# Optimization experiments

Measured on AMD Instinct MI355X. Metric: run time of the kernel, lower is better.

The kernel has to match this reference:

```python
import jax, jax.numpy as jnp
import numpy as np

N_FRAMES = 4
HEADS = 8
SEQ = 576
DIM = 640


def setup_inputs() -> dict:
    key = jax.random.key(0)
    ks = jax.random.split(key, 6)
    x = jax.random.normal(ks[0], (3 * N_FRAMES, SEQ, DIM), dtype=jnp.float32)
    s = 1.0 / np.sqrt(DIM)
    Wq = jax.random.normal(ks[1], (DIM, DIM), dtype=jnp.float32) * s
    Wk = jax.random.normal(ks[2], (DIM, DIM), dtype=jnp.float32) * s
    Wv = jax.random.normal(ks[3], (DIM, DIM), dtype=jnp.float32) * s
    Wo = jax.random.normal(ks[4], (DIM, DIM), dtype=jnp.float32) * s
    bo = jnp.zeros((DIM,), dtype=jnp.float32)
    return {"x": x, "Wq": Wq, "Wk": Wk, "Wv": Wv, "Wo": Wo, "bo": bo}


def reference(x, Wq, Wk, Wv, Wo, bo):
    # x: [3F, S, D] -- stacked [source | uncond | cond] frame batches
    B, S, D = x.shape
    n = B // 3                       # n_frames
    h = HEADS
    hd = D // h
    scale = 1.0 / jnp.sqrt(jnp.asarray(hd, x.dtype))

    # torch nn.Linear: y = x @ W.T
    q = jnp.einsum('bsd,ed->bse', x, Wq)
    k = jnp.einsum('bsd,ed->bse', x, Wk)
    v = jnp.einsum('bsd,ed->bse', x, Wv)

    def heads_fd(t):  # [F,S,D] -> [F,h,S,hd]
        return t.reshape(t.shape[0], S, h, hd).transpose(0, 2, 1, 3)

    def heads_flat(t):  # [F,S,D] -> [h, F*S, hd]  (shared across all query frames)
        return t.reshape(t.shape[0] * S, h, hd).transpose(1, 0, 2)

    # ---- source: per-frame self-attention ----
    qs, ks_, vs = heads_fd(q[:n]), heads_fd(k[:n]), heads_fd(v[:n])
    sim_s = jnp.einsum('fhqd,fhkd->fhqk', qs, ks_) * scale
    out_s = jnp.einsum('fhqk,fhkd->fhqd', jax.nn.softmax(sim_s, axis=-1), vs)

    # ---- uncond / cond: each frame attends to concatenated KV of all frames ----
    def cross_frame(q_chunk, k_chunk, v_chunk):
        qf = heads_fd(q_chunk)          # [F,h,S,hd]
        kf = heads_flat(k_chunk)        # [h,F*S,hd]
        vf = heads_flat(v_chunk)        # [h,F*S,hd]
        sim = jnp.einsum('fhqd,hkd->fhqk', qf, kf) * scale   # [F,h,S,F*S]
        return jnp.einsum('fhqk,hkd->fhqd', jax.nn.softmax(sim, axis=-1), vf)

    out_u = cross_frame(q[n:2 * n], k[n:2 * n], v[n:2 * n])
    out_c = cross_frame(q[2 * n:], k[2 * n:], v[2 * n:])

    out = jnp.concatenate([out_s, out_u, out_c], axis=0)      # [3F,h,S,hd]
    out = out.transpose(0, 2, 1, 3).reshape(B, S, D)          # merge heads
    return jnp.einsum('bsd,ed->bse', out, Wo) + bo
```

## Files before the change

kernel.cpp:

```cpp
#include <hip/hip_runtime.h>
#include <hip/hip_bf16.h>

#define SEQ    576
#define DIM    640
#define HEADS  8
#define HD     80
#define NF     4
#define NB     12
#define M_TOT  (NB * SEQ)
#define SCALE  0.11180339887498949f
#define LOG2E  1.4426950408889634f

typedef __attribute__((ext_vector_type(8))) short          bf16x8;
typedef __attribute__((ext_vector_type(4))) float          f32x4;
typedef __attribute__((ext_vector_type(8))) unsigned short u16x8;
typedef __attribute__((ext_vector_type(4))) unsigned short u16x4;

__device__ __forceinline__ unsigned short f2bf(float x) {
    unsigned u = __float_as_uint(x);
    u += 0x7fffu + ((u >> 16) & 1u);
    return (unsigned short)(u >> 16);
}
__device__ __forceinline__ float bf2f(unsigned short h) {
    return __uint_as_float((unsigned)h << 16);
}
__device__ __forceinline__ f32x4 mfma16(bf16x8 a, bf16x8 b, f32x4 c) {
    return __builtin_amdgcn_mfma_f32_16x16x32_bf16(a, b, c, 0, 0, 0);
}
__device__ __forceinline__ float fexp2(float x) {
    return __builtin_amdgcn_exp2f(x);
}
__device__ __forceinline__ void dma16(const void* g, void* s) {
    __builtin_amdgcn_global_load_lds(
        (const __attribute__((address_space(1))) void*)g,
        (__attribute__((address_space(3))) void*)s, 16, 0, 0);
}

__global__ __launch_bounds__(256) void split_kernel(
    const float* __restrict__ X,  const float* __restrict__ Wq,
    const float* __restrict__ Wk, const float* __restrict__ Wv,
    const float* __restrict__ Wo,
    unsigned short* __restrict__ Xh,  unsigned short* __restrict__ Wqh,
    unsigned short* __restrict__ Wkh, unsigned short* __restrict__ Wvh,
    unsigned short* __restrict__ Woh)
{
    const int z = blockIdx.y;
    const float* src; unsigned short* dh; int n; float s = 1.0f;
    switch (z) {
        case 0:  src = X;  dh = Xh;  n = M_TOT * DIM; break;
        case 1:  src = Wq; dh = Wqh; n = DIM * DIM; s = SCALE * LOG2E; break;
        case 2:  src = Wk; dh = Wkh; n = DIM * DIM; break;
        case 3:  src = Wv; dh = Wvh; n = DIM * DIM; break;
        default: src = Wo; dh = Woh; n = DIM * DIM; break;
    }
    const int base = blockIdx.x * 4096 + threadIdx.x * 16;
    if (base >= n) return;
#pragma unroll
    for (int half = 0; half < 2; ++half) {
        const int b = base + half * 8;
        float4 a4 = *(const float4*)(src + b);
        float4 b4 = *(const float4*)(src + b + 4);
        float vv[8] = {a4.x, a4.y, a4.z, a4.w, b4.x, b4.y, b4.z, b4.w};
        union { unsigned short u[8]; u16x8 v; } ph;
#pragma unroll
        for (int j = 0; j < 8; ++j) ph.u[j] = f2bf(vv[j] * s);
        *(u16x8*)(dh + b) = ph.v;
    }
}

__global__ __launch_bounds__(256) void qkv_mfma_kernel(
    const unsigned short* __restrict__ Xh,
    const unsigned short* __restrict__ Wqh, const unsigned short* __restrict__ Wkh,
    const unsigned short* __restrict__ Wvh,
    unsigned short* __restrict__ Qh,
    unsigned short* __restrict__ Kb, unsigned short* __restrict__ VtG)
{
    __shared__ unsigned short smem[10240];
    unsigned short* As = smem;
    unsigned short* Bs = smem + 8192;

    const int flat = blockIdx.x + 27 * (blockIdx.y + 10 * blockIdx.z);
    const int xcd  = flat & 7;
    const int slot = flat >> 3;
    const int l    = (xcd < 2 ? xcd * 102 : 204 + (xcd - 2) * 101) + slot;
    const int m_idx = l / 30;
    const int rem   = l - m_idx * 30;
    const int z     = rem / 10;
    const int n_idx = rem - z * 10;

    const unsigned short* WH = (z == 0) ? Wqh : ((z == 1) ? Wkh : Wvh);
    const int m0 = m_idx * 256;
    const int n0 = n_idx * 64;

    const int t    = threadIdx.x;
    const int w    = t >> 6;
    const int lane = t & 63;
    const int quad = lane >> 4;
    const int ln   = lane & 15;

    f32x4 acc[4][4];
#pragma unroll
    for (int mi = 0; mi < 4; ++mi)
#pragma unroll
        for (int nt = 0; nt < 4; ++nt)
#pragma unroll
            for (int e = 0; e < 4; ++e) acc[mi][nt][e] = 0.f;

    const int lr = lane >> 2;
    const int lc = (lane & 3) * 8;

    for (int k0 = 0; k0 < DIM; k0 += 32) {
        __syncthreads();
        {
            const unsigned short* gp = Xh + (size_t)(m0 + w * 64 + lr) * DIM + k0 + lc;
#pragma unroll
            for (int i = 0; i < 4; ++i)
                dma16(gp + (size_t)i * 16 * DIM, &As[(w * 64 + i * 16) * 32]);
            const size_t gb = (size_t)(n0 + w * 16 + lr) * DIM + k0 + lc;
            dma16(WH + gb, &Bs[w * 16 * 32]);
        }
        __syncthreads();

        bf16x8 af[4];
#pragma unroll
        for (int mi = 0; mi < 4; ++mi)
            af[mi] = *(const bf16x8*)&As[(w * 64 + mi * 16 + ln) * 32 + quad * 8];
#pragma unroll
        for (int nt = 0; nt < 4; ++nt) {
            bf16x8 bh = *(const bf16x8*)&Bs[(nt * 16 + ln) * 32 + quad * 8];
#pragma unroll
            for (int mi = 0; mi < 4; ++mi)
                acc[mi][nt] = mfma16(af[mi], bh, acc[mi][nt]);
        }
    }

    if (z == 0) {
#pragma unroll
        for (int mi = 0; mi < 4; ++mi)
#pragma unroll
            for (int r = 0; r < 4; ++r) {
                const size_t row = m0 + w * 64 + mi * 16 + quad * 4 + r;
#pragma unroll
                for (int nt = 0; nt < 4; ++nt)
                    Qh[row * DIM + n0 + nt * 16 + ln] = f2bf(acc[mi][nt][r]);
            }
    } else if (z == 1) {
#pragma unroll
        for (int mi = 0; mi < 4; ++mi)
#pragma unroll
            for (int r = 0; r < 4; ++r) {
                const size_t row = m0 + w * 64 + mi * 16 + quad * 4 + r;
#pragma unroll
                for (int nt = 0; nt < 4; ++nt)
                    Kb[row * DIM + n0 + nt * 16 + ln] = f2bf(acc[mi][nt][r]);
            }
    } else {
        unsigned short* Vts = smem;
#pragma unroll 1
        for (int half = 0; half < 2; ++half) {
            __syncthreads();
            if ((w >> 1) == half) {
                const int wl = w & 1;
#pragma unroll
                for (int mi = 0; mi < 4; ++mi)
#pragma unroll
                    for (int nt = 0; nt < 4; ++nt)
#pragma unroll
                        for (int r = 0; r < 4; ++r)
                            Vts[(nt * 16 + ln) * 136 + wl * 64 + mi * 16 + quad * 4 + r] =
                                f2bf(acc[mi][nt][r]);
            }
            __syncthreads();
            const int nn = t & 63;
            const int c0 = (t >> 6) * 32;
#pragma unroll
            for (int i = 0; i < 4; ++i)
                *(u16x8*)(VtG + (size_t)(n0 + nn) * M_TOT + m0 + half * 128 + c0 + i * 8) =
                    *(const u16x8*)&Vts[nn * 136 + c0 + i * 8];
        }
    }
}

__global__ __launch_bounds__(256, 2) void attn_mfma_kernel(
    const unsigned short* __restrict__ Qh,
    const unsigned short* __restrict__ Kb, const unsigned short* __restrict__ Vt,
    unsigned short* __restrict__ Oh,
    unsigned short* __restrict__ Pn, float2* __restrict__ ml)
{
    const int flat = blockIdx.x + 3 * (blockIdx.y + 8 * blockIdx.z);
    const int h    = flat & 7;
    const int slot = flat >> 3;
    const int z    = slot / 3;
    const int qt   = slot - z * 3;

    int f, kbase, nkt, idx = -1;
    if (z < 16) {
        idx = z;
        const int fi = z >> 1;
        f = 4 + fi;
        kbase = ((fi < 4 ? 4 : 8) + (z & 1) * 2) * SEQ;
        nkt = 18;
    } else {
        f = z - 16;
        kbase = f * SEQ;
        nkt = 9;
    }

    const int t    = threadIdx.x;
    const int w    = t >> 6;
    const int lane = t & 63;
    const int quad = lane >> 4;
    const int ln   = lane & 15;

    __shared__ unsigned short KhS[64 * 96];
    __shared__ unsigned short VtS[80 * 64];
    __shared__ unsigned short Pb[4 * 48 * 72];

    bf16x8 qf[3][3];
#pragma unroll
    for (int mi = 0; mi < 3; ++mi) {
        const int qrow = f * SEQ + qt * 192 + w * 48 + mi * 16 + ln;
        const unsigned short* qp = Qh + (size_t)qrow * DIM + h * HD;
#pragma unroll
        for (int kc = 0; kc < 3; ++kc) {
            const int dbase = kc * 32 + quad * 8;
            if (dbase < HD) {
                qf[mi][kc] = *(const bf16x8*)(qp + dbase);
            } else {
                union { unsigned short u[8]; bf16x8 v; } zz;
#pragma unroll
                for (int j = 0; j < 8; ++j) zz.u[j] = 0;
                qf[mi][kc] = zz.v;
            }
        }
    }

    float m_[3], l_[3];
#pragma unroll
    for (int mi = 0; mi < 3; ++mi) { m_[mi] = -INFINITY; l_[mi] = 0.f; }

    f32x4 oacc[3][5];
#pragma unroll
    for (int mi = 0; mi < 3; ++mi)
#pragma unroll
        for (int nt = 0; nt < 5; ++nt)
#pragma unroll
            for (int e = 0; e < 4; ++e) oacc[mi][nt][e] = 0.f;

    unsigned short* PbW = &Pb[w * 48 * 72];

    for (int kt = 0; kt < nkt; ++kt) {
        __syncthreads();
        {
            const unsigned short* kg = Kb + (size_t)(kbase + kt * 64) * DIM + h * HD;
#pragma unroll
            for (int rnd = 0; rnd < 3; ++rnd) {
                const int unit = rnd * 256 + t;
                const int kr = unit / 12, kc = unit % 12;
                dma16(kg + (size_t)kr * DIM + kc * 8,
                      &KhS[(rnd * 256 + w * 64) * 8]);
            }
        }
        {
#pragma unroll
            for (int u = t; u < 640; u += 256) {
                const int d = u >> 3, c8 = u & 7;
                const int c8s = (c8 + 3 * d) & 7;
                *(u16x8*)&VtS[d * 64 + c8s * 8] =
                    *(const u16x8*)(Vt + (size_t)(h * HD + d) * M_TOT +
                                    kbase + kt * 64 + c8 * 8);
            }
        }
        __syncthreads();

        f32x4 sacc[3][4];
#pragma unroll
        for (int mi = 0; mi < 3; ++mi)
#pragma unroll
            for (int nt = 0; nt < 4; ++nt)
#pragma unroll
                for (int e = 0; e < 4; ++e) sacc[mi][nt][e] = 0.f;
#pragma unroll
        for (int nt = 0; nt < 4; ++nt)
#pragma unroll
            for (int kc = 0; kc < 3; ++kc) {
                bf16x8 kf = *(const bf16x8*)&KhS[(nt * 16 + ln) * 96 + kc * 32 + quad * 8];
#pragma unroll
                for (int mi = 0; mi < 3; ++mi)
                    sacc[mi][nt] = mfma16(kf, qf[mi][kc], sacc[mi][nt]);
            }

        float aq[3];
#pragma unroll
        for (int mi = 0; mi < 3; ++mi) {
            float mx = sacc[mi][0][0];
#pragma unroll
            for (int nt = 0; nt < 4; ++nt)
#pragma unroll
                for (int r = 0; r < 4; ++r) mx = fmaxf(mx, sacc[mi][nt][r]);
            mx = fmaxf(mx, __shfl_xor(mx, 16));
            mx = fmaxf(mx, __shfl_xor(mx, 32));
            const float mnew = fmaxf(m_[mi], mx);
            aq[mi] = fexp2(m_[mi] - mnew);
            m_[mi] = mnew;
            float s = 0.f;
#pragma unroll
            for (int nt = 0; nt < 4; ++nt) {
                union { unsigned short u[4]; u16x4 v; } pk;
#pragma unroll
                for (int r = 0; r < 4; ++r) {
                    const float p = fexp2(sacc[mi][nt][r] - m_[mi]);
                    s += p;
                    pk.u[r] = (unsigned short)(__float_as_uint(p) >> 16);
                }
                *(u16x4*)&PbW[(mi * 16 + ln) * 72 + nt * 16 + quad * 4] = pk.v;
            }
            s += __shfl_xor(s, 16);
            s += __shfl_xor(s, 32);
            l_[mi] = l_[mi] * aq[mi] + s;
        }

#pragma unroll
        for (int mi = 0; mi < 3; ++mi)
#pragma unroll
            for (int r = 0; r < 4; ++r) {
                const float ar = __shfl(aq[mi], quad * 4 + r, 64);
#pragma unroll
                for (int nt = 0; nt < 5; ++nt) oacc[mi][nt][r] *= ar;
            }

        __threadfence_block();

#pragma unroll
        for (int kc = 0; kc < 2; ++kc) {
            bf16x8 pf[3];
#pragma unroll
            for (int mi = 0; mi < 3; ++mi)
                pf[mi] = *(const bf16x8*)&PbW[(mi * 16 + ln) * 72 + kc * 32 + quad * 8];
#pragma unroll
            for (int nt = 0; nt < 5; ++nt) {
                const int vrow = nt * 16 + ln;
                const int c8r  = ((kc * 4 + quad) + 3 * vrow) & 7;
                bf16x8 vf = *(const bf16x8*)&VtS[vrow * 64 + c8r * 8];
#pragma unroll
                for (int mi = 0; mi < 3; ++mi)
                    oacc[mi][nt] = mfma16(pf[mi], vf, oacc[mi][nt]);
            }
        }
    }

#pragma unroll
    for (int mi = 0; mi < 3; ++mi)
#pragma unroll
        for (int r = 0; r < 4; ++r) {
            const float lr_ = __shfl(l_[mi], quad * 4 + r, 64);
            const float inv = 1.f / lr_;
            const int rr = qt * 192 + w * 48 + mi * 16 + quad * 4 + r;
            if (idx < 0) {
                const size_t orow = (size_t)f * SEQ + rr;
#pragma unroll
                for (int nt = 0; nt < 5; ++nt)
                    Oh[orow * DIM + h * HD + nt * 16 + ln] = f2bf(oacc[mi][nt][r] * inv);
            } else {
#pragma unroll
                for (int nt = 0; nt < 5; ++nt)
                    Pn[((size_t)idx * SEQ + rr) * DIM + h * HD + nt * 16 + ln] =
                        f2bf(oacc[mi][nt][r] * inv);
            }
        }
    if (idx >= 0 && lane < 16) {
#pragma unroll
        for (int mi = 0; mi < 3; ++mi) {
            const int rr = qt * 192 + w * 48 + mi * 16 + lane;
            ml[((size_t)idx * 8 + h) * SEQ + rr] = make_float2(m_[mi], l_[mi]);
        }
    }
}

__global__ __launch_bounds__(320) void merge_kernel(
    const unsigned short* __restrict__ Pn, const float2* __restrict__ ml,
    unsigned short* __restrict__ Oh)
{
    const int row = blockIdx.x;
    const int fi  = blockIdx.y;
    const int t   = threadIdx.x;
    const int i0  = fi * 2, i1 = i0 + 1;
#pragma unroll
    for (int rep = 0; rep < 2; ++rep) {
        const int col = t + rep * 320;
        const int h = col / 80;
        const float2 a = ml[((size_t)i0 * 8 + h) * SEQ + row];
        const float2 b = ml[((size_t)i1 * 8 + h) * SEQ + row];
        const float M  = fmaxf(a.x, b.x);
        const float w0 = fexp2(a.x - M) * a.y;
        const float w1 = fexp2(b.x - M) * b.y;
        const float inv = 1.f / (w0 + w1);
        const float p0 = bf2f(Pn[((size_t)i0 * SEQ + row) * DIM + col]);
        const float p1 = bf2f(Pn[((size_t)i1 * SEQ + row) * DIM + col]);
        Oh[((size_t)(4 + fi) * SEQ + row) * DIM + col] = f2bf((w0 * p0 + w1 * p1) * inv);
    }
}

__global__ __launch_bounds__(256) void oproj_mfma_kernel(
    const unsigned short* __restrict__ Oh,
    const unsigned short* __restrict__ Woh,
    const float* __restrict__ bo, float* __restrict__ out)
{
    __shared__ unsigned short smem[10240];
    unsigned short* As = smem;
    unsigned short* Bs = smem + 8192;

    const int flat = blockIdx.x + 27 * blockIdx.y;
    const int xcd  = flat & 7;
    const int slot = flat >> 3;
    const int l    = (xcd < 6 ? xcd * 34 : 204 + (xcd - 6) * 33) + slot;
    const int m_idx = l / 10;
    const int n_idx = l - m_idx * 10;
    const int m0 = m_idx * 256;
    const int n0 = n_idx * 64;

    const int t    = threadIdx.x;
    const int w    = t >> 6;
    const int lane = t & 63;
    const int quad = lane >> 4;
    const int ln   = lane & 15;

    f32x4 acc[4][4];
#pragma unroll
    for (int mi = 0; mi < 4; ++mi)
#pragma unroll
        for (int nt = 0; nt < 4; ++nt)
#pragma unroll
            for (int e = 0; e < 4; ++e) acc[mi][nt][e] = 0.f;

    const int lr = lane >> 2;
    const int lc = (lane & 3) * 8;

    for (int k0 = 0; k0 < DIM; k0 += 32) {
        __syncthreads();
        {
            const unsigned short* gp = Oh + (size_t)(m0 + w * 64 + lr) * DIM + k0 + lc;
#pragma unroll
            for (int i = 0; i < 4; ++i)
                dma16(gp + (size_t)i * 16 * DIM, &As[(w * 64 + i * 16) * 32]);
            const size_t gb = (size_t)(n0 + w * 16 + lr) * DIM + k0 + lc;
            dma16(Woh + gb, &Bs[w * 16 * 32]);
        }
        __syncthreads();

        bf16x8 af[4];
#pragma unroll
        for (int mi = 0; mi < 4; ++mi)
            af[mi] = *(const bf16x8*)&As[(w * 64 + mi * 16 + ln) * 32 + quad * 8];
#pragma unroll
        for (int nt = 0; nt < 4; ++nt) {
            bf16x8 bh = *(const bf16x8*)&Bs[(nt * 16 + ln) * 32 + quad * 8];
#pragma unroll
            for (int mi = 0; mi < 4; ++mi)
                acc[mi][nt] = mfma16(af[mi], bh, acc[mi][nt]);
        }
    }

#pragma unroll
    for (int mi = 0; mi < 4; ++mi)
#pragma unroll
        for (int r = 0; r < 4; ++r) {
            const size_t row = m0 + w * 64 + mi * 16 + quad * 4 + r;
#pragma unroll
            for (int nt = 0; nt < 4; ++nt) {
                const int col = n0 + nt * 16 + ln;
                out[row * DIM + col] = acc[mi][nt][r] + bo[col];
            }
        }
}

extern "C" void kernel_launch(void* const* d_in, const int* in_sizes, int n_in,
                              void* d_out, int out_size, void* d_ws, size_t ws_size,
                              hipStream_t stream)
{
    const float* x  = (const float*)d_in[0];
    const float* Wq = (const float*)d_in[1];
    const float* Wk = (const float*)d_in[2];
    const float* Wv = (const float*)d_in[3];
    const float* Wo = (const float*)d_in[4];
    const float* bo = (const float*)d_in[5];
    float* out = (float*)d_out;

    const size_t NX = (size_t)M_TOT * DIM;
    const size_t NW = (size_t)DIM * DIM;
    unsigned short* p = (unsigned short*)d_ws;
    unsigned short* Wqh = p;  p += NW;
    unsigned short* Wkh = p;  p += NW;
    unsigned short* Wvh = p;  p += NW;
    unsigned short* Woh = p;  p += NW;
    unsigned short* Xh  = p;  p += NX;
    unsigned short* Qhb = p;  p += NX;
    unsigned short* Kbb = p;  p += NX;
    unsigned short* Vtb = p;  p += NX;
    unsigned short* Ohb = Xh;

    unsigned short* Pn = (unsigned short*)d_out;
    float2* ml = (float2*)((char*)d_out + (size_t)16 * SEQ * DIM * 2);

    dim3 g0((unsigned)((NX + 4095) / 4096), 5);
    split_kernel<<<g0, 256, 0, stream>>>(x, Wq, Wk, Wv, Wo,
        Xh, Wqh, Wkh, Wvh, Woh);

    dim3 g1(M_TOT / 256, DIM / 64, 3);
    qkv_mfma_kernel<<<g1, 256, 0, stream>>>(Xh, Wqh, Wkh, Wvh, Qhb, Kbb, Vtb);

    dim3 g2(3, HEADS, 20);
    attn_mfma_kernel<<<g2, 256, 0, stream>>>(Qhb, Kbb, Vtb, Ohb, Pn, ml);

    dim3 g3(SEQ, 8);
    merge_kernel<<<g3, 320, 0, stream>>>(Pn, ml, Ohb);

    dim3 g4(M_TOT / 256, DIM / 64);
    oproj_mfma_kernel<<<g4, 256, 0, stream>>>(Ohb, Woh, bo, out);
}
```

Before: 201.1 us.

## Double-buffer LDS tiles in QKV, attention, and output-projection kernels

Adds two-stage shared-memory buffering to the QKV and output-projection GEMMs: the next K-slice is issued by async DMA while MFMAs run on the current one, which removes one barrier per iteration. The attention kernel also double-buffers its K and V tiles. K is prefetched by DMA, and V is loaded into registers early and written to the alternate LDS buffer after the PV MFMAs. The aim is to hide global-load latency behind compute. The cost is more LDS per block and more registers for the V prefetch, which may reduce occupancy.

```diff
diff --git a/kernel.cpp b/kernel.cpp
--- a/kernel.cpp
+++ b/kernel.cpp
@@ -75,9 +75,7 @@
     unsigned short* __restrict__ Qh,
     unsigned short* __restrict__ Kb, unsigned short* __restrict__ VtG)
 {
-    __shared__ unsigned short smem[10240];
-    unsigned short* As = smem;
-    unsigned short* Bs = smem + 8192;
+    __shared__ unsigned short smem[2][10240];
 
     const int flat = blockIdx.x + 27 * (blockIdx.y + 10 * blockIdx.z);
     const int xcd  = flat & 7;
@@ -109,18 +107,26 @@
     const int lr = lane >> 2;
     const int lc = (lane & 3) * 8;
 
+    auto stage = [&](int buf, int k0) {
+        unsigned short* As = smem[buf];
+        unsigned short* Bs = smem[buf] + 8192;
+        const unsigned short* gp = Xh + (size_t)(m0 + w * 64 + lr) * DIM + k0 + lc;
+#pragma unroll
+        for (int i = 0; i < 4; ++i)
+            dma16(gp + (size_t)i * 16 * DIM, &As[(w * 64 + i * 16) * 32]);
+        const size_t gb = (size_t)(n0 + w * 16 + lr) * DIM + k0 + lc;
+        dma16(WH + gb, &Bs[w * 16 * 32]);
+    };
+
+    stage(0, 0);
+    __syncthreads();
+
     for (int k0 = 0; k0 < DIM; k0 += 32) {
-        __syncthreads();
-        {
-            const unsigned short* gp = Xh + (size_t)(m0 + w * 64 + lr) * DIM + k0 + lc;
-#pragma unroll
-            for (int i = 0; i < 4; ++i)
-                dma16(gp + (size_t)i * 16 * DIM, &As[(w * 64 + i * 16) * 32]);
-            const size_t gb = (size_t)(n0 + w * 16 + lr) * DIM + k0 + lc;
-            dma16(WH + gb, &Bs[w * 16 * 32]);
-        }
-        __syncthreads();
-
+        const int kb = (k0 >> 5) & 1;
+        if (k0 + 32 < DIM) stage(kb ^ 1, k0 + 32);
+
+        const unsigned short* As = smem[kb];
+        const unsigned short* Bs = smem[kb] + 8192;
         bf16x8 af[4];
 #pragma unroll
         for (int mi = 0; mi < 4; ++mi)
@@ -132,6 +138,7 @@
             for (int mi = 0; mi < 4; ++mi)
                 acc[mi][nt] = mfma16(af[mi], bh, acc[mi][nt]);
         }
+        __syncthreads();
     }
 
     if (z == 0) {
@@ -155,7 +162,7 @@
                     Kb[row * DIM + n0 + nt * 16 + ln] = f2bf(acc[mi][nt][r]);
             }
     } else {
-        unsigned short* Vts = smem;
+        unsigned short* Vts = smem[0];
 #pragma unroll 1
         for (int half = 0; half < 2; ++half) {
             __syncthreads();
@@ -212,8 +219,8 @@
     const int quad = lane >> 4;
     const int ln   = lane & 15;
 
-    __shared__ unsigned short KhS[64 * 96];
-    __shared__ unsigned short VtS[80 * 64];
+    __shared__ unsigned short KhS[2][64 * 96];
+    __shared__ unsigned short VtS[2][80 * 64];
     __shared__ unsigned short Pb[4 * 48 * 72];
 
     bf16x8 qf[3][3];
@@ -235,43 +242,67 @@
         }
     }
 
-    float m_[3], l_[3];
-#pragma unroll
-    for (int mi = 0; mi < 3; ++mi) { m_[mi] = -INFINITY; l_[mi] = 0.f; }
-
-    f32x4 oacc[3][5];
-#pragma unroll
-    for (int mi = 0; mi < 3; ++mi)
-#pragma unroll
-        for (int nt = 0; nt < 5; ++nt)
-#pragma unroll
-            for (int e = 0; e < 4; ++e) oacc[mi][nt][e] = 0.f;
-
-    unsigned short* PbW = &Pb[w * 48 * 72];
-
-    for (int kt = 0; kt < nkt; ++kt) {
-        __syncthreads();
-        {
-            const unsigned short* kg = Kb + (size_t)(kbase + kt * 64) * DIM + h * HD;
-#pragma unroll
-            for (int rnd = 0; rnd < 3; ++rnd) {
-                const int unit = rnd * 256 + t;
-                const int kr = unit / 12, kc = unit % 12;
-                dma16(kg + (size_t)kr * DIM + kc * 8,
-                      &KhS[(rnd * 256 + w * 64) * 8]);
-            }
-        }
-        {
-#pragma unroll
-            for (int u = t; u < 640; u += 256) {
+    auto stage_k = [&](int buf, int kvt) {
+        const unsigned short* kg = Kb + (size_t)(kbase + kvt * 64) * DIM + h * HD;
+#pragma unroll
+        for (int rnd = 0; rnd < 3; ++rnd) {
+            const int unit = rnd * 256 + t;
+            const int kr = unit / 12, kc = unit % 12;
+            dma16(kg + (size_t)kr * DIM + kc * 8,
+                  &KhS[buf][(rnd * 256 + w * 64) * 8]);
+        }
+    };
+    u16x8 vreg[3];
+    auto load_v = [&](int kvt) {
+#pragma unroll
+        for (int i = 0; i < 3; ++i) {
+            const int u = t + i * 256;
+            if (u < 640) {
+                const int d = u >> 3, c8 = u & 7;
+                vreg[i] = *(const u16x8*)(Vt + (size_t)(h * HD + d) * M_TOT +
+                                          kbase + kvt * 64 + c8 * 8);
+            }
+        }
+    };
+    auto write_v = [&](int buf) {
+#pragma unroll
+        for (int i = 0; i < 3; ++i) {
+            const int u = t + i * 256;
+            if (u < 640) {
                 const int d = u >> 3, c8 = u & 7;
                 const int c8s = (c8 + 3 * d) & 7;
-                *(u16x8*)&VtS[d * 64 + c8s * 8] =
-                    *(const u16x8*)(Vt + (size_t)(h * HD + d) * M_TOT +
-                                    kbase + kt * 64 + c8 * 8);
-            }
-        }
-        __syncthreads();
+                *(u16x8*)&VtS[buf][d * 64 + c8s * 8] = vreg[i];
+            }
+        }
+    };
+
+    float m_[3], l_[3];
+#pragma unroll
+    for (int mi = 0; mi < 3; ++mi) { m_[mi] = -INFINITY; l_[mi] = 0.f; }
+
+    f32x4 oacc[3][5];
+#pragma unroll
+    for (int mi = 0; mi < 3; ++mi)
+#pragma unroll
+        for (int nt = 0; nt < 5; ++nt)
+#pragma unroll
+            for (int e = 0; e < 4; ++e) oacc[mi][nt][e] = 0.f;
+
+    unsigned short* PbW = &Pb[w * 48 * 72];
+
+    stage_k(0, 0);
+    load_v(0);
+    write_v(0);
+    __syncthreads();
+
+    for (int kt = 0; kt < nkt; ++kt) {
+        const int cur = kt & 1;
+        const bool pf = (kt + 1 < nkt);
+
+        if (pf) {
+            load_v(kt + 1);
+            stage_k(cur ^ 1, kt + 1);
+        }
 
         f32x4 sacc[3][4];
 #pragma unroll
@@ -284,7 +315,7 @@
         for (int nt = 0; nt < 4; ++nt)
 #pragma unroll
             for (int kc = 0; kc < 3; ++kc) {
-                bf16x8 kf = *(const bf16x8*)&KhS[(nt * 16 + ln) * 96 + kc * 32 + quad * 8];
+                bf16x8 kf = *(const bf16x8*)&KhS[cur][(nt * 16 + ln) * 96 + kc * 32 + quad * 8];
 #pragma unroll
                 for (int mi = 0; mi < 3; ++mi)
                     sacc[mi][nt] = mfma16(kf, qf[mi][kc], sacc[mi][nt]);
@@ -333,20 +364,23 @@
 
 #pragma unroll
         for (int kc = 0; kc < 2; ++kc) {
-            bf16x8 pf[3];
+            bf16x8 pf_[3];
 #pragma unroll
             for (int mi = 0; mi < 3; ++mi)
-                pf[mi] = *(const bf16x8*)&PbW[(mi * 16 + ln) * 72 + kc * 32 + quad * 8];
+                pf_[mi] = *(const bf16x8*)&PbW[(mi * 16 + ln) * 72 + kc * 32 + quad * 8];
 #pragma unroll
             for (int nt = 0; nt < 5; ++nt) {
                 const int vrow = nt * 16 + ln;
                 const int c8r  = ((kc * 4 + quad) + 3 * vrow) & 7;
-                bf16x8 vf = *(const bf16x8*)&VtS[vrow * 64 + c8r * 8];
+                bf16x8 vf = *(const bf16x8*)&VtS[cur][vrow * 64 + c8r * 8];
 #pragma unroll
                 for (int mi = 0; mi < 3; ++mi)
-                    oacc[mi][nt] = mfma16(pf[mi], vf, oacc[mi][nt]);
-            }
-        }
+                    oacc[mi][nt] = mfma16(pf_[mi], vf, oacc[mi][nt]);
+            }
+        }
+
+        if (pf) write_v(cur ^ 1);
+        __syncthreads();
     }
 
 #pragma unroll
@@ -406,9 +440,7 @@
     const unsigned short* __restrict__ Woh,
     const float* __restrict__ bo, float* __restrict__ out)
 {
-    __shared__ unsigned short smem[10240];
-    unsigned short* As = smem;
-    unsigned short* Bs = smem + 8192;
+    __shared__ unsigned short smem[2][10240];
 
     const int flat = blockIdx.x + 27 * blockIdx.y;
     const int xcd  = flat & 7;
@@ -436,18 +468,26 @@
     const int lr = lane >> 2;
     const int lc = (lane & 3) * 8;
 
+    auto stage = [&](int buf, int k0) {
+        unsigned short* As = smem[buf];
+        unsigned short* Bs = smem[buf] + 8192;
+        const unsigned short* gp = Oh + (size_t)(m0 + w * 64 + lr) * DIM + k0 + lc;
+#pragma unroll
+        for (int i = 0; i < 4; ++i)
+            dma16(gp + (size_t)i * 16 * DIM, &As[(w * 64 + i * 16) * 32]);
+        const size_t gb = (size_t)(n0 + w * 16 + lr) * DIM + k0 + lc;
+        dma16(Woh + gb, &Bs[w * 16 * 32]);
+    };
+
+    stage(0, 0);
+    __syncthreads();
+
     for (int k0 = 0; k0 < DIM; k0 += 32) {
-        __syncthreads();
-        {
-            const unsigned short* gp = Oh + (size_t)(m0 + w * 64 + lr) * DIM + k0 + lc;
-#pragma unroll
-            for (int i = 0; i < 4; ++i)
-                dma16(gp + (size_t)i * 16 * DIM, &As[(w * 64 + i * 16) * 32]);
-            const size_t gb = (size_t)(n0 + w * 16 + lr) * DIM + k0 + lc;
-            dma16(Woh + gb, &Bs[w * 16 * 32]);
-        }
-        __syncthreads();
-
+        const int kb = (k0 >> 5) & 1;
+        if (k0 + 32 < DIM) stage(kb ^ 1, k0 + 32);
+
+        const unsigned short* As = smem[kb];
+        const unsigned short* Bs = smem[kb] + 8192;
         bf16x8 af[4];
 #pragma unroll
         for (int mi = 0; mi < 4; ++mi)
@@ -459,6 +499,7 @@
             for (int mi = 0; mi < 4; ++mi)
                 acc[mi][nt] = mfma16(af[mi], bh, acc[mi][nt]);
         }
+        __syncthreads();
     }
 
 #pragma unroll
```

New measurement: 193.3 us. 3.9% less time.
